# Kernel tuning notes

Hardware: AMD Instinct MI355X
Metric: run time of the kernel (lower is better)

Reference implementation:

```python
import jax, jax.numpy as jnp
import numpy as np
from jax import lax

L = 8
PATCH = 3
DIRS = [(0, 1), (1, 0), (1, 1), (1, -1)]


def _pair_indices():
    coords = np.arange(PATCH * PATCH)
    rr, cc = coords // PATCH, coords % PATCH
    i1s, i2s = [], []
    for dr, dc in DIRS:
        m = (rr + dr >= 0) & (rr + dr < PATCH) & (cc + dc >= 0) & (cc + dc < PATCH)
        i1s.append(coords[m])
        i2s.append((rr[m] + dr) * PATCH + (cc[m] + dc))
    return np.concatenate(i1s), np.concatenate(i2s)

_I1, _I2 = _pair_indices()


def conv_bn_silu(x, w, s, b, pad):
    # Conv2d(bias=False) + eval-mode BatchNorm folded into (s, b) + SiLU
    y = lax.conv_general_dilated(x, w, (1, 1), [(pad, pad), (pad, pad)],
                                 dimension_numbers=("NCHW", "OIHW", "NCHW"))
    y = y * s[None, :, None, None] + b[None, :, None, None]
    return jax.nn.silu(y)


def glcm_feats(x):
    B, C, H, W = x.shape
    pad = PATCH // 2
    xp = jnp.pad(x, ((0, 0), (0, 0), (pad, pad), (pad, pad)), mode="edge")
    # unfold: (B, C, 9, H, W)
    patches = jnp.stack([xp[:, :, i:i + H, j:j + W]
                         for i in range(PATCH) for j in range(PATCH)], axis=2)
    q = jnp.clip((patches * (L - 1)).astype(jnp.int32), 0, L - 1)
    q = q.reshape(B * C, PATCH * PATCH, H * W)
    # co-occurrence pair indices for all 4 directions, concatenated: (BC, K, HW)
    idx = q[:, _I1, :] * L + q[:, _I2, :]
    idx = idx.transpose(0, 2, 1)  # (BC, HW, K)
    # per-pixel local histogram over L*L bins (scatter-add)
    hist = jax.vmap(jax.vmap(
        lambda v: jnp.zeros((L * L,), x.dtype).at[v].add(1.0)))(idx)
    hist = hist / len(DIRS)  # reduce_mode='average'
    s = jnp.maximum(hist.sum(-1, keepdims=True), 1e-6)
    p = hist / s  # (BC, HW, L*L)
    li = jnp.arange(L, dtype=x.dtype)
    diff = li[:, None] - li[None, :]
    diff_sq = (diff ** 2).reshape(-1)
    abs_d = jnp.abs(diff).reshape(-1)
    contrast = (p * diff_sq).sum(-1)
    energy = (p * p).sum(-1)
    entropy = -(p * jnp.log(p + 1e-6)).sum(-1)
    homog = (p / (1.0 + abs_d)).sum(-1)
    f = jnp.stack([contrast, energy, entropy, homog], axis=-1)  # (BC, HW, 4)
    f = f.reshape(B, C, H * W, 4).mean(axis=1)  # average over channels
    return f.transpose(0, 2, 1).reshape(B, 4, H, W)


def setup_inputs() -> dict:
    key = jax.random.key(0)
    B, C, H, W = 4, 64, 80, 80
    c_, cb, c2 = 32, 16, 64
    ks = iter(jax.random.split(key, 20))
    x = jax.random.uniform(next(ks), (B, C, H, W), jnp.float32)

    def conv_p(cin, cout, ksz):
        w = jax.random.normal(next(ks), (cout, cin, ksz, ksz), jnp.float32) / np.sqrt(cin * ksz * ksz)
        s = jax.random.uniform(next(ks), (cout,), jnp.float32, 0.5, 1.5)
        b = jax.random.normal(next(ks), (cout,), jnp.float32) * 0.1
        return w, s, b

    cv1_w, cv1_s, cv1_b = conv_p(C + 4, c_, 1)
    cv2_w, cv2_s, cv2_b = conv_p(C + 4, c_, 1)
    m1_w, m1_s, m1_b = conv_p(c_, cb, 1)
    m2_w, m2_s, m2_b = conv_p(cb, c_, 3)
    cv3_w, cv3_s, cv3_b = conv_p(2 * c_, c2, 1)
    return dict(x=x, cv1_w=cv1_w, cv1_s=cv1_s, cv1_b=cv1_b,
                cv2_w=cv2_w, cv2_s=cv2_s, cv2_b=cv2_b,
                m1_w=m1_w, m1_s=m1_s, m1_b=m1_b,
                m2_w=m2_w, m2_s=m2_s, m2_b=m2_b,
                cv3_w=cv3_w, cv3_s=cv3_s, cv3_b=cv3_b)


def reference(x, cv1_w, cv1_s, cv1_b, cv2_w, cv2_s, cv2_b,
              m1_w, m1_s, m1_b, m2_w, m2_s, m2_b,
              cv3_w, cv3_s, cv3_b):
    g = glcm_feats(x)
    xc = jnp.concatenate([x, g], axis=1)  # (B, C+4, H, W)
    a = conv_bn_silu(xc, cv1_w, cv1_s, cv1_b, 0)
    y = conv_bn_silu(a, m1_w, m1_s, m1_b, 0)
    y = conv_bn_silu(y, m2_w, m2_s, m2_b, 1)
    a = a + y  # Bottleneck shortcut (c1 == c2)
    b = conv_bn_silu(xc, cv2_w, cv2_s, cv2_b, 0)
    return conv_bn_silu(jnp.concatenate([a, b], axis=1), cv3_w, cv3_s, cv3_b, 0)
```

## Files before the change

kernel.cpp:

```cpp
#include <hip/hip_runtime.h>
#include <math.h>

constexpr int B = 4, C = 64, H = 80, W = 80;
constexpr int HW = H * W;
constexpr int NPIX = B * HW;
constexpr int PXB = 16;

typedef unsigned u32;

static __device__ __forceinline__ float silu(float v) {
    float e = __expf(-v);
    return v * __builtin_amdgcn_rcpf(1.0f + e);
}

static __device__ __forceinline__ u32 pks(u32 a, u32 b){u32 d; asm("v_pk_sub_u16 %0,%1,%2":"=v"(d):"v"(a),"v"(b)); return d;}
static __device__ __forceinline__ u32 pka(u32 a, u32 b){u32 d; asm("v_pk_add_u16 %0,%1,%2":"=v"(d):"v"(a),"v"(b)); return d;}
static __device__ __forceinline__ u32 pkm(u32 a, u32 b){u32 d; asm("v_pk_mul_lo_u16 %0,%1,%2":"=v"(d):"v"(a),"v"(b)); return d;}
static __device__ __forceinline__ u32 pkmin(u32 a, u32 b){u32 d; asm("v_pk_min_u16 %0,%1,%2":"=v"(d):"v"(a),"v"(b)); return d;}
static __device__ __forceinline__ u32 pkmaxi(u32 a, u32 b){u32 d; asm("v_pk_max_i16 %0,%1,%2":"=v"(d):"v"(a),"v"(b)); return d;}
static __device__ __forceinline__ float cb0(u32 a){float f; asm("v_cvt_f32_ubyte0 %0,%1":"=v"(f):"v"(a)); return f;}
static __device__ __forceinline__ float cb2(u32 a){float f; asm("v_cvt_f32_ubyte2 %0,%1":"=v"(f):"v"(a)); return f;}

static __device__ __forceinline__ void ce(u32 &x, u32 &y) {
    u32 mn, mx;
    asm("v_pk_min_u16 %0, %2, %3\n\t"
        "v_pk_max_u16 %1, %2, %3"
        : "=&v"(mn), "=v"(mx) : "v"(x), "v"(y));
    x = mn; y = mx;
}

__global__ __launch_bounds__(512, 4) void glcm_stage1_kernel(
    const float* __restrict__ x,
    const float* __restrict__ w1, const float* __restrict__ s1, const float* __restrict__ b1,
    const float* __restrict__ w2, const float* __restrict__ s2, const float* __restrict__ b2,
    const float* __restrict__ wm1, const float* __restrict__ sm1, const float* __restrict__ bm1,
    float* __restrict__ a, float* __restrict__ bbuf, float* __restrict__ y16) {
    __shared__ float ws1T[68 * 33];
    __shared__ float ws2T[68 * 33];
    __shared__ float wsm1T[32 * 17];
    __shared__ float xs[68][PXB];
    __shared__ float aT[32][PXB];
    __shared__ float red[8][PXB][4];

    const int t = threadIdx.x;

    {
        const int oc = t >> 4, i0 = t & 15;
        #pragma unroll
        for (int ic = i0; ic < 68; ic += 16) {
            ws1T[ic * 33 + oc] = w1[oc * 68 + ic];
            ws2T[ic * 33 + oc] = w2[oc * 68 + ic];
        }
        if (oc < 16) {
            wsm1T[i0 * 17 + oc]        = wm1[oc * 32 + i0];
            wsm1T[(i0 + 16) * 17 + oc] = wm1[oc * 32 + i0 + 16];
        }
    }

    const int pxl = t & 15;
    const int grp = t >> 4;
    const int pix = blockIdx.x * PXB + pxl;
    const int b = pix / HW;
    const int hw = pix - b * HW;
    const int h = hw / W;
    const int w = hw - h * W;
    const int hm = h > 0 ? h - 1 : 0;
    const int hp = h < H - 1 ? h + 1 : H - 1;
    const int wm = w > 0 ? w - 1 : 0;
    const int wp = w < W - 1 ? w + 1 : W - 1;
    const int o[9] = {hm * W + wm, hm * W + w, hm * W + wp,
                      h  * W + wm, h  * W + w, h  * W + wp,
                      hp * W + wm, hp * W + w, hp * W + wp};
    const float* c0 = x + (size_t)(b * C + grp * 2) * HW;
    const float* c1 = c0 + HW;

    u32 qpk[9];
    #pragma unroll
    for (int k = 0; k < 9; ++k) {
        const float v0 = c0[o[k]];
        const float v1 = c1[o[k]];
        if (k == 4) {
            xs[grp * 2][pxl] = v0;
            xs[grp * 2 + 1][pxl] = v1;
        }
        int a0 = (int)(v0 * 7.0f);
        int a1 = (int)(v1 * 7.0f);
        a0 = a0 < 0 ? 0 : (a0 > 7 ? 7 : a0);
        a1 = a1 < 0 ? 0 : (a1 > 7 ? 7 : a1);
        qpk[k] = (u32)a0 | ((u32)a1 << 16);
    }

    static constexpr int PA[20] = {0,1,3,4,6,7, 0,1,2,3,4,5, 0,1,3,4, 1,2,4,5};
    static constexpr int PB[20] = {1,2,4,5,7,8, 3,4,5,6,7,8, 4,5,7,8, 3,4,6,7};

    const u32 ONEpk = 0x00010001u, EIGHTpk = 0x00080008u;
    u32 cs = 0;
    float hsum = 0.f;
    u32 key[20];
    #pragma unroll
    for (int ai = 0; ai < 20; ++ai) {
        const u32 qa = qpk[PA[ai]], qb = qpk[PB[ai]];
        const u32 d = pks(qa, qb);
        cs = pka(cs, pkm(d, d));
        const u32 ad = pkmaxi(d, pks(0u, d));
        const u32 h1 = pka(ad, ONEpk);
        hsum += __builtin_amdgcn_rcpf(cb0(h1)) + __builtin_amdgcn_rcpf(cb2(h1));
        key[ai] = pka(pkm(qa, EIGHTpk), qb);
    }

    #pragma unroll
    for (int p = 1; p < 32; p <<= 1) {
        #pragma unroll
        for (int k = p; k >= 1; k >>= 1) {
            const int jm = k % p;
            #pragma unroll
            for (int lo = 0; lo < 20; ++lo) {
                const int hi = lo + k;
                if (hi < 20 && lo >= jm && ((lo - jm) % (2 * k)) < k &&
                    (lo / (2 * p)) == (hi / (2 * p))) {
                    ce(key[lo], key[hi]);
                }
            }
        }
    }

    u32 eq[20];
    #pragma unroll
    for (int ai = 1; ai < 20; ++ai)
        eq[ai] = pks(ONEpk, pkmin(pks(key[ai], key[ai - 1]), ONEpk));

    u32 pc = 0, ps = 0, pv[20];
    pv[0] = 0;
    #pragma unroll
    for (int ai = 1; ai < 20; ++ai) {
        pc = pkm(pka(pc, ONEpk), eq[ai]);
        pv[ai] = pc;
        ps = pka(ps, pc);
    }
    float pr0, pr1;
    {
        const u32 m = pka(pv[19], ONEpk);
        pr0 = cb0(m); pr1 = cb2(m);
    }
    u32 rc = 0;
    #pragma unroll
    for (int ai = 18; ai >= 0; --ai) {
        rc = pkm(pka(rc, ONEpk), eq[ai + 1]);
        const u32 m = pka(pka(pv[ai], rc), ONEpk);
        pr0 *= cb0(m); pr1 *= cb2(m);
    }

    const int csum = (int)(cs & 0xFFFFu) + (int)(cs >> 16);
    const int psum = (int)(ps & 0xFFFFu) + (int)(ps >> 16);
    const float lsum = __logf(pr0) + __logf(pr1);

    float fc = (float)csum * (1.f / 20.f);
    float fe = ((float)psum * 2.f + 40.f) * (1.f / 400.f);
    float fn = -(lsum + 40.f * -2.9957322736f) * (1.f / 20.f);
    float fh = hsum * (1.f / 20.f);

    fc += __shfl_xor(fc, 16); fe += __shfl_xor(fe, 16);
    fn += __shfl_xor(fn, 16); fh += __shfl_xor(fh, 16);
    fc += __shfl_xor(fc, 32); fe += __shfl_xor(fe, 32);
    fn += __shfl_xor(fn, 32); fh += __shfl_xor(fh, 32);
    const int wv = t >> 6;
    if ((t & 63) < 16) {
        red[wv][pxl][0] = fc; red[wv][pxl][1] = fe;
        red[wv][pxl][2] = fn; red[wv][pxl][3] = fh;
    }
    __syncthreads();
    if (t < 64) {
        const int p2 = t >> 2, f = t & 3;
        float s = 0.f;
        #pragma unroll
        for (int wq = 0; wq < 8; ++wq) s += red[wq][p2][f];
        xs[64 + f][p2] = s * (1.f / 64.f);
    }
    __syncthreads();

    {
        const int px = t & 15;
        const int oc = t >> 4;
        float acc1 = 0.f, acc2 = 0.f;
        #pragma unroll 4
        for (int ic = 0; ic < 68; ++ic) {
            const float v = xs[ic][px];
            acc1 += v * ws1T[ic * 33 + oc];
            acc2 += v * ws2T[ic * 33 + oc];
        }
        const int pix2 = blockIdx.x * PXB + px;
        const int bb = pix2 / HW;
        const int hw2 = pix2 - bb * HW;
        const float v1 = silu(acc1 * s1[oc] + b1[oc]);
        a[((size_t)(bb * 32 + oc)) * HW + hw2] = v1;
        aT[oc][px] = v1;
        bbuf[((size_t)(bb * 32 + oc)) * HW + hw2] = silu(acc2 * s2[oc] + b2[oc]);
    }
    __syncthreads();

    if (t < 256) {
        const int px = t & 15;
        const int oc = t >> 4;
        float acc = 0.f;
        #pragma unroll 4
        for (int ic = 0; ic < 32; ++ic)
            acc += aT[ic][px] * wsm1T[ic * 17 + oc];
        const int pix2 = blockIdx.x * PXB + px;
        const int bb = pix2 / HW;
        const int hw2 = pix2 - bb * HW;
        y16[((size_t)(bb * 16 + oc)) * HW + hw2] = silu(acc * sm1[oc] + bm1[oc]);
    }
}

__global__ __launch_bounds__(512) void m2cv3_kernel(
    const float* __restrict__ y16, const float* __restrict__ a,
    const float* __restrict__ bbuf,
    const float* __restrict__ wm2, const float* __restrict__ sm2, const float* __restrict__ bm2,
    const float* __restrict__ wc, const float* __restrict__ sc, const float* __restrict__ bc,
    float* __restrict__ out) {
    __shared__ float ys[16][4][82];
    __shared__ float a2[32][64];
    __shared__ float bs[32][64];
    const int t = threadIdx.x;
    const int p0 = blockIdx.x * 64;
    const int bi = p0 / HW;
    const int hw0 = p0 - bi * HW;
    const int h0 = hw0 / W;

    const float* yb = y16 + (size_t)(bi * 16) * HW;
    for (int e = t; e < 16 * 4 * 82; e += 512) {
        const int ch = e / 328;
        const int rem = e - ch * 328;
        const int row = rem / 82;
        const int col = rem - row * 82;
        const int r = h0 - 1 + row;
        const int c = col - 1;
        float v = 0.f;
        if ((unsigned)r < (unsigned)H && (unsigned)c < (unsigned)W)
            v = yb[(size_t)ch * HW + r * W + c];
        ys[ch][row][col] = v;
    }
    for (int e = t; e < 32 * 64; e += 512) {
        const int ic = e >> 6, px = e & 63;
        bs[ic][px] = bbuf[((size_t)(bi * 32 + ic)) * HW + hw0 + px];
    }
    __syncthreads();

    const int lane = t & 63;
    const int wv = __builtin_amdgcn_readfirstlane(t >> 6);
    const int hw = hw0 + lane;
    const int h = hw / W;
    const int w = hw - h * W;
    const int lr = h - h0;
    const int oc0 = wv * 4;

    float acc[4] = {0.f, 0.f, 0.f, 0.f};
    #pragma unroll 2
    for (int ic = 0; ic < 16; ++ic) {
        #pragma unroll
        for (int ky = 0; ky < 3; ++ky) {
            #pragma unroll
            for (int kx = 0; kx < 3; ++kx) {
                const float v = ys[ic][lr + ky][w + kx];
                const int tap = ic * 9 + ky * 3 + kx;
                #pragma unroll
                for (int j = 0; j < 4; ++j)
                    acc[j] += v * wm2[(oc0 + j) * 144 + tap];
            }
        }
    }
    #pragma unroll
    for (int j = 0; j < 4; ++j) {
        const int oc = oc0 + j;
        a2[oc][lane] = a[((size_t)(bi * 32 + oc)) * HW + hw]
                     + silu(acc[j] * sm2[oc] + bm2[oc]);
    }
    __syncthreads();
    const int oc3 = wv * 8;
    float c_[8] = {0.f, 0.f, 0.f, 0.f, 0.f, 0.f, 0.f, 0.f};
    #pragma unroll 4
    for (int ic = 0; ic < 32; ++ic) {
        const float av = a2[ic][lane];
        const float bv = bs[ic][lane];
        #pragma unroll
        for (int j = 0; j < 8; ++j) {
            c_[j] += av * wc[(oc3 + j) * 64 + ic];
            c_[j] += bv * wc[(oc3 + j) * 64 + 32 + ic];
        }
    }
    #pragma unroll
    for (int j = 0; j < 8; ++j) {
        const int oc = oc3 + j;
        out[((size_t)(bi * 64 + oc)) * HW + hw] = silu(c_[j] * sc[oc] + bc[oc]);
    }
}

extern "C" void kernel_launch(void* const* d_in, const int* in_sizes, int n_in,
                              void* d_out, int out_size, void* d_ws, size_t ws_size,
                              hipStream_t stream) {
    const float* x    = (const float*)d_in[0];
    const float* cv1w = (const float*)d_in[1];
    const float* cv1s = (const float*)d_in[2];
    const float* cv1b = (const float*)d_in[3];
    const float* cv2w = (const float*)d_in[4];
    const float* cv2s = (const float*)d_in[5];
    const float* cv2b = (const float*)d_in[6];
    const float* m1w  = (const float*)d_in[7];
    const float* m1s  = (const float*)d_in[8];
    const float* m1b  = (const float*)d_in[9];
    const float* m2w  = (const float*)d_in[10];
    const float* m2s  = (const float*)d_in[11];
    const float* m2b  = (const float*)d_in[12];
    const float* cv3w = (const float*)d_in[13];
    const float* cv3s = (const float*)d_in[14];
    const float* cv3b = (const float*)d_in[15];

    float* ws   = (float*)d_ws;
    float* a    = ws;
    float* bbuf = ws + 819200;
    float* y16  = ws + 1638400;

    glcm_stage1_kernel<<<NPIX / PXB, 512, 0, stream>>>(
        x, cv1w, cv1s, cv1b, cv2w, cv2s, cv2b, m1w, m1s, m1b, a, bbuf, y16);
    m2cv3_kernel<<<NPIX / 64, 512, 0, stream>>>(y16, a, bbuf, m2w, m2s, m2b,
                                                cv3w, cv3s, cv3b, (float*)d_out);
}
```

Measured before the change: 60.20 us.

## Stage quantized 3x18 halo tile in LDS and vectorize 1x1 conv weight reads

The GLCM stage now loads each 16-pixel strip's 3x18 halo once per channel pair into shared memory, quantizing on load, so threads no longer issue nine separate global gathers per pixel. The conv weights are copied untransposed with float4 loads, and the input/weight tiles are laid out pixel-major so the 68-channel dot products use float4 LDS reads. Batch and row indices are computed once per block, which assumes a 16-pixel block never straddles an image row. That holds because W=80 is a multiple of 16. It adds an extra barrier and more shared memory, which may lower occupancy.

```diff
diff --git a/kernel.cpp b/kernel.cpp
--- a/kernel.cpp
+++ b/kernel.cpp
@@ -35,60 +35,56 @@
     const float* __restrict__ w2, const float* __restrict__ s2, const float* __restrict__ b2,
     const float* __restrict__ wm1, const float* __restrict__ sm1, const float* __restrict__ bm1,
     float* __restrict__ a, float* __restrict__ bbuf, float* __restrict__ y16) {
-    __shared__ float ws1T[68 * 33];
-    __shared__ float ws2T[68 * 33];
-    __shared__ float wsm1T[32 * 17];
-    __shared__ float xs[68][PXB];
-    __shared__ float aT[32][PXB];
+    __shared__ u32 qcell[32][3][18];
+    __shared__ __align__(16) float xs[PXB][72];
+    __shared__ __align__(16) float ws1[32][68];
+    __shared__ __align__(16) float ws2[32][68];
+    __shared__ __align__(16) float wsm1[16][32];
+    __shared__ float aT[PXB][33];
     __shared__ float red[8][PXB][4];
 
     const int t = threadIdx.x;
+    const int p0g = blockIdx.x * PXB;
+    const int bb  = p0g / HW;
+    const int hw0 = p0g - bb * HW;
+    const int h0  = hw0 / W;
+    const int c0g = hw0 - h0 * W;
 
     {
-        const int oc = t >> 4, i0 = t & 15;
-        #pragma unroll
-        for (int ic = i0; ic < 68; ic += 16) {
-            ws1T[ic * 33 + oc] = w1[oc * 68 + ic];
-            ws2T[ic * 33 + oc] = w2[oc * 68 + ic];
-        }
-        if (oc < 16) {
-            wsm1T[i0 * 17 + oc]        = wm1[oc * 32 + i0];
-            wsm1T[(i0 + 16) * 17 + oc] = wm1[oc * 32 + i0 + 16];
-        }
-    }
+        const float4* w1f = (const float4*)w1;
+        const float4* w2f = (const float4*)w2;
+        float4* s1f = (float4*)&ws1[0][0];
+        float4* s2f = (float4*)&ws2[0][0];
+        for (int e = t; e < 544; e += 512) { s1f[e] = w1f[e]; s2f[e] = w2f[e]; }
+        if (t < 128) ((float4*)&wsm1[0][0])[t] = ((const float4*)wm1)[t];
+    }
+    for (int e = t; e < 32 * 3 * 18; e += 512) {
+        const int grp = e / 54;
+        const int rem = e - grp * 54;
+        const int row = rem / 18;
+        const int col = rem - row * 18;
+        int gr = h0 + row - 1;  gr = gr < 0 ? 0 : (gr > H - 1 ? H - 1 : gr);
+        int gc = c0g + col - 1; gc = gc < 0 ? 0 : (gc > W - 1 ? W - 1 : gc);
+        const float v0 = x[((size_t)(bb * C + grp * 2)) * HW + gr * W + gc];
+        const float v1 = x[((size_t)(bb * C + grp * 2 + 1)) * HW + gr * W + gc];
+        int q0 = (int)(v0 * 7.0f); q0 = q0 < 0 ? 0 : (q0 > 7 ? 7 : q0);
+        int q1 = (int)(v1 * 7.0f); q1 = q1 < 0 ? 0 : (q1 > 7 ? 7 : q1);
+        qcell[grp][row][col] = (u32)q0 | ((u32)q1 << 16);
+        if (row == 1 && col >= 1 && col <= 16) {
+            xs[col - 1][grp * 2]     = v0;
+            xs[col - 1][grp * 2 + 1] = v1;
+        }
+    }
+    __syncthreads();
 
     const int pxl = t & 15;
     const int grp = t >> 4;
-    const int pix = blockIdx.x * PXB + pxl;
-    const int b = pix / HW;
-    const int hw = pix - b * HW;
-    const int h = hw / W;
-    const int w = hw - h * W;
-    const int hm = h > 0 ? h - 1 : 0;
-    const int hp = h < H - 1 ? h + 1 : H - 1;
-    const int wm = w > 0 ? w - 1 : 0;
-    const int wp = w < W - 1 ? w + 1 : W - 1;
-    const int o[9] = {hm * W + wm, hm * W + w, hm * W + wp,
-                      h  * W + wm, h  * W + w, h  * W + wp,
-                      hp * W + wm, hp * W + w, hp * W + wp};
-    const float* c0 = x + (size_t)(b * C + grp * 2) * HW;
-    const float* c1 = c0 + HW;
-
     u32 qpk[9];
     #pragma unroll
-    for (int k = 0; k < 9; ++k) {
-        const float v0 = c0[o[k]];
-        const float v1 = c1[o[k]];
-        if (k == 4) {
-            xs[grp * 2][pxl] = v0;
-            xs[grp * 2 + 1][pxl] = v1;
-        }
-        int a0 = (int)(v0 * 7.0f);
-        int a1 = (int)(v1 * 7.0f);
-        a0 = a0 < 0 ? 0 : (a0 > 7 ? 7 : a0);
-        a1 = a1 < 0 ? 0 : (a1 > 7 ? 7 : a1);
-        qpk[k] = (u32)a0 | ((u32)a1 << 16);
-    }
+    for (int r = 0; r < 3; ++r)
+        #pragma unroll
+        for (int k = 0; k < 3; ++k)
+            qpk[r * 3 + k] = qcell[grp][r][pxl + k];
 
     static constexpr int PA[20] = {0,1,3,4,6,7, 0,1,2,3,4,5, 0,1,3,4, 1,2,4,5};
     static constexpr int PB[20] = {1,2,4,5,7,8, 3,4,5,6,7,8, 4,5,7,8, 3,4,6,7};
@@ -174,7 +170,7 @@
         float s = 0.f;
         #pragma unroll
         for (int wq = 0; wq < 8; ++wq) s += red[wq][p2][f];
-        xs[64 + f][p2] = s * (1.f / 64.f);
+        xs[p2][64 + f] = s * (1.f / 64.f);
     }
     __syncthreads();
 
@@ -182,18 +178,18 @@
         const int px = t & 15;
         const int oc = t >> 4;
         float acc1 = 0.f, acc2 = 0.f;
-        #pragma unroll 4
-        for (int ic = 0; ic < 68; ++ic) {
-            const float v = xs[ic][px];
-            acc1 += v * ws1T[ic * 33 + oc];
-            acc2 += v * ws2T[ic * 33 + oc];
-        }
-        const int pix2 = blockIdx.x * PXB + px;
-        const int bb = pix2 / HW;
-        const int hw2 = pix2 - bb * HW;
+        #pragma unroll
+        for (int k = 0; k < 17; ++k) {
+            const float4 xv = *reinterpret_cast<const float4*>(&xs[px][k * 4]);
+            const float4 wa = *reinterpret_cast<const float4*>(&ws1[oc][k * 4]);
+            const float4 wb = *reinterpret_cast<const float4*>(&ws2[oc][k * 4]);
+            acc1 += xv.x * wa.x + xv.y * wa.y + xv.z * wa.z + xv.w * wa.w;
+            acc2 += xv.x * wb.x + xv.y * wb.y + xv.z * wb.z + xv.w * wb.w;
+        }
+        const int hw2 = hw0 + px;
         const float v1 = silu(acc1 * s1[oc] + b1[oc]);
         a[((size_t)(bb * 32 + oc)) * HW + hw2] = v1;
-        aT[oc][px] = v1;
+        aT[px][oc] = v1;
         bbuf[((size_t)(bb * 32 + oc)) * HW + hw2] = silu(acc2 * s2[oc] + b2[oc]);
     }
     __syncthreads();
@@ -202,13 +198,10 @@
         const int px = t & 15;
         const int oc = t >> 4;
         float acc = 0.f;
-        #pragma unroll 4
+        #pragma unroll 8
         for (int ic = 0; ic < 32; ++ic)
-            acc += aT[ic][px] * wsm1T[ic * 17 + oc];
-        const int pix2 = blockIdx.x * PXB + px;
-        const int bb = pix2 / HW;
-        const int hw2 = pix2 - bb * HW;
-        y16[((size_t)(bb * 16 + oc)) * HW + hw2] = silu(acc * sm1[oc] + bm1[oc]);
+            acc += aT[px][ic] * wsm1[oc][ic];
+        y16[((size_t)(bb * 16 + oc)) * HW + hw0 + px] = silu(acc * sm1[oc] + bm1[oc]);
     }
 }
 
```

After: 61.49 us. +2.1%, slower.
